# Kernel tuning notes

Measured on AMD Instinct MI355X. Metric: run time of the kernel, lower is better.

Reference implementation:

```python
import jax, jax.numpy as jnp
import numpy as np

DIM = 1024      # dim
FW = 14         # focal_window
FL = 2          # focal_level
FF = 4          # focal_factor


def _dwconv_gelu(x, w, b):
    # x: [B, C, S], w: [C, 1, k] depthwise kernel, torch 'same' padding
    k = w.shape[-1]
    y = jax.lax.conv_general_dilated(
        x, w, window_strides=(1,), padding=[((k - 1) // 2, k // 2)],
        feature_group_count=x.shape[1], dimension_numbers=('NCH', 'OIH', 'NCH'))
    return jax.nn.gelu(y + b[None, :, None], approximate=False)


def setup_inputs() -> dict:
    key = jax.random.key(0)
    ks = jax.random.split(key, 8)
    B, S, D = 8, 4096, DIM
    P = 2 * D + FL + 1  # 2051
    s = 0.02
    return {
        'input': jax.random.normal(ks[0], (B, S, D), jnp.float32),
        'W_in': jax.random.normal(ks[1], (D, P), jnp.float32) * s,
        'b_in': jnp.zeros((P,), jnp.float32),
        'w0': jax.random.normal(ks[2], (D, 1, FW), jnp.float32) * s,
        'b0': jnp.zeros((D,), jnp.float32),
        'w1': jax.random.normal(ks[3], (D, 1, FF + FW), jnp.float32) * s,  # kernel 18
        'b1': jnp.zeros((D,), jnp.float32),
        'W_ctx': jax.random.normal(ks[4], (D, D), jnp.float32) * s,
        'b_ctx': jnp.zeros((D,), jnp.float32),
        'W_out': jax.random.normal(ks[5], (D, D), jnp.float32) * s,
        'b_out': jnp.zeros((D,), jnp.float32),
    }


def reference(input, W_in, b_in, w0, b0, w1, b1, W_ctx, b_ctx, W_out, b_out):
    D = DIM
    # in_proj then permute to channel-first [B, 2D+FL+1, S]
    proj = (input @ W_in + b_in).transpose(0, 2, 1)
    query = proj[:, :D]            # [B, D, S]
    ctx = proj[:, D:2 * D]         # [B, D, S]
    gates = proj[:, 2 * D:]        # [B, FL+1, S]
    # hierarchical depthwise conv pyramid (context fed through successive levels)
    c0 = _dwconv_gelu(ctx, w0, b0)
    c1 = _dwconv_gelu(c0, w1, b1)
    context_all = c0 * gates[:, 0:1] + c1 * gates[:, 1:2]
    # global context branch
    g = jax.nn.gelu(c1.mean(axis=-1), approximate=False)  # [B, D]
    context_all = context_all + g[..., None] * gates[:, FL:FL + 1]
    # context_proj is a 1x1 conv == per-position linear over channels
    modulator = jnp.einsum('oc,bcs->bos', W_ctx, context_all) + b_ctx[None, :, None]
    out = (query * modulator).transpose(0, 2, 1)  # [B, S, D]
    return out @ W_out + b_out
```

## Files before the change

kernel.cpp:

```cpp
#include <hip/hip_runtime.h>

#define DIMC 1024
#define BATCH 8
#define SEQ 4096
#define BS (BATCH*SEQ)
#define PCOL 2051

typedef unsigned short ushort_t;
typedef __attribute__((ext_vector_type(8))) short short8;
typedef __attribute__((ext_vector_type(4))) float f32x4;
typedef __attribute__((ext_vector_type(4))) unsigned short us4;

__device__ __forceinline__ float bf2f(ushort_t u) {
    union { unsigned u32; float f; } v; v.u32 = ((unsigned)u) << 16; return v.f;
}
__device__ __forceinline__ ushort_t f2bf(float f) {
    union { float f; unsigned u; } v; v.f = f;
    unsigned r = v.u + 0x7fffu + ((v.u >> 16) & 1u);
    return (ushort_t)(r >> 16);
}
__device__ __forceinline__ float gelu_exact(float x) {
    return 0.5f * x * (1.0f + erff(x * 0.7071067811865475f));
}
__device__ __forceinline__ void gld16(const ushort_t* g, ushort_t* l) {
    __builtin_amdgcn_global_load_lds(
        (const __attribute__((address_space(1))) unsigned int*)g,
        (__attribute__((address_space(3))) unsigned int*)l, 16, 0, 0);
}

__global__ void cvt_f32_bf16(const float* __restrict__ src, ushort_t* __restrict__ dst, int n) {
    int i = (blockIdx.x * 256 + threadIdx.x) * 4;
    if (i >= n) return;
    f32x4 v = *(const f32x4*)(src + i);
    us4 o;
    #pragma unroll
    for (int j = 0; j < 4; j++) o[j] = f2bf(v[j]);
    *(us4*)(dst + i) = o;
}

__global__ void transpose_cvt(const float* __restrict__ src, ushort_t* __restrict__ dst,
                              int ld, int K) {
    __shared__ float tile[32][33];
    int tx = threadIdx.x & 31, ty = threadIdx.x >> 5;
    int n0 = blockIdx.x * 32, k0 = blockIdx.y * 32;
    #pragma unroll
    for (int j = 0; j < 4; j++)
        tile[ty + j * 8][tx] = src[(size_t)(k0 + ty + j * 8) * ld + n0 + tx];
    __syncthreads();
    #pragma unroll
    for (int j = 0; j < 4; j++)
        dst[(size_t)(n0 + ty + j * 8) * K + k0 + tx] = f2bf(tile[tx][ty + j * 8]);
}

__global__ void pack_gatesw(const float* __restrict__ W_in, float* __restrict__ wg) {
    int d = blockIdx.x * 256 + threadIdx.x;
    if (d >= 1024) return;
    const float* p = W_in + (size_t)d * PCOL + 2048;
    wg[d] = p[0]; wg[1024 + d] = p[1]; wg[2048 + d] = p[2];
}

__global__ void cvt_gates(const float* __restrict__ input, const float* __restrict__ wg,
                          const float* __restrict__ b_in, ushort_t* __restrict__ ibf,
                          float* __restrict__ gates) {
    int row = blockIdx.x, tid = threadIdx.x;
    int lane = tid & 63, wave = tid >> 6;
    size_t base = (size_t)row * 1024 + tid * 4;
    f32x4 v = *(const f32x4*)(input + base);
    us4 o;
    #pragma unroll
    for (int j = 0; j < 4; j++) o[j] = f2bf(v[j]);
    *(us4*)(ibf + base) = o;
    f32x4 w0v = *(const f32x4*)(wg + tid * 4);
    f32x4 w1v = *(const f32x4*)(wg + 1024 + tid * 4);
    f32x4 w2v = *(const f32x4*)(wg + 2048 + tid * 4);
    float a0 = 0, a1 = 0, a2 = 0;
    #pragma unroll
    for (int j = 0; j < 4; j++) { a0 += v[j] * w0v[j]; a1 += v[j] * w1v[j]; a2 += v[j] * w2v[j]; }
    #pragma unroll
    for (int off = 32; off; off >>= 1) {
        a0 += __shfl_down(a0, off, 64);
        a1 += __shfl_down(a1, off, 64);
        a2 += __shfl_down(a2, off, 64);
    }
    __shared__ float red[4][3];
    if (lane == 0) { red[wave][0] = a0; red[wave][1] = a1; red[wave][2] = a2; }
    __syncthreads();
    if (tid == 0) {
        gates[row * 4 + 0] = red[0][0] + red[1][0] + red[2][0] + red[3][0] + b_in[2048];
        gates[row * 4 + 1] = red[0][1] + red[1][1] + red[2][1] + red[3][1] + b_in[2049];
        gates[row * 4 + 2] = red[0][2] + red[1][2] + red[2][2] + red[3][2] + b_in[2050];
    }
}

template<int MODE>
__global__ __launch_bounds__(512, 2)
void gemm256(const ushort_t* __restrict__ A, const ushort_t* __restrict__ Bt,
             const float* __restrict__ bias, void* __restrict__ C,
             const ushort_t* __restrict__ Q, const float* __restrict__ gates,
             const float* __restrict__ vb, int K, int ldc, int ldq, int nbx) {
    __shared__ ushort_t lA[2][16384];
    __shared__ ushort_t lB[2][16384];
    const int tid = threadIdx.x, lane = tid & 63, wave = tid >> 6;
    const int lr = lane & 15, kq = lane >> 4;
    const int wrm = wave >> 2, wrn = wave & 3;

    const int nwg = gridDim.x, bid = blockIdx.x;
    const int q8 = nwg >> 3, r8 = nwg & 7;
    const int xcd = bid & 7, linb = bid >> 3;
    const int wgid = (xcd < r8 ? xcd * (q8 + 1) : r8 * (q8 + 1) + (xcd - r8) * q8) + linb;
    const int bn = wgid % nbx, bm = wgid / nbx;

    const ushort_t* Ag = A + (size_t)bm * 256 * K;
    const ushort_t* Bg = Bt + (size_t)bn * 256 * K;

    const int xsw = kq ^ (((lr >> 3) & 1) << 1);
    const int fBase = lr * 32 + xsw * 8;

    int srOff[2][2], ldsC[2][2];
    #pragma unroll
    for (int h = 0; h < 2; h++)
        #pragma unroll
        for (int j = 0; j < 2; j++) {
            int c = h * 1024 + j * 512 + tid;
            int sub = c >> 6, rl = (c >> 2) & 15, cc = c & 3;
            int r  = ((sub >> 1) << 4) | rl;
            int k8 = ((sub & 1) << 2) | (cc ^ (((rl >> 3) & 1) << 1));
            srOff[h][j] = r * K + k8 * 8;
            ldsC[h][j]  = (h * 1024 + j * 512 + (wave << 6)) << 3;
        }

    f32x4 acc[8][4];
    #pragma unroll
    for (int i = 0; i < 8; i++)
        #pragma unroll
        for (int j = 0; j < 4; j++)
            #pragma unroll
            for (int r = 0; r < 4; r++) acc[i][j][r] = 0.f;

    short8 af[2][2], bfr[4][2];

#define STG(ARR, bb, G, kt, h) do { \
    gld16((G) + (size_t)(kt) * 64 + srOff[h][0], &ARR[bb][ldsC[h][0]]); \
    gld16((G) + (size_t)(kt) * 64 + srOff[h][1], &ARR[bb][ldsC[h][1]]); \
} while (0)

#define PHASE(bb, qq, STAGE_STMT, DOVM) do { \
    if ((qq) == 0) { \
        _Pragma("unroll") \
        for (int nt = 0; nt < 4; nt++) { \
            bfr[nt][0] = *(const short8*)&lB[bb][fBase + ((wrn * 4 + nt) * 2 + 0) * 512]; \
            bfr[nt][1] = *(const short8*)&lB[bb][fBase + ((wrn * 4 + nt) * 2 + 1) * 512]; \
        } \
    } \
    af[0][0] = *(const short8*)&lA[bb][fBase + ((wrm * 8 + (qq) * 2 + 0) * 2 + 0) * 512]; \
    af[0][1] = *(const short8*)&lA[bb][fBase + ((wrm * 8 + (qq) * 2 + 0) * 2 + 1) * 512]; \
    af[1][0] = *(const short8*)&lA[bb][fBase + ((wrm * 8 + (qq) * 2 + 1) * 2 + 0) * 512]; \
    af[1][1] = *(const short8*)&lA[bb][fBase + ((wrm * 8 + (qq) * 2 + 1) * 2 + 1) * 512]; \
    STAGE_STMT; \
    __builtin_amdgcn_s_barrier(); \
    asm volatile("s_waitcnt lgkmcnt(0)" ::: "memory"); \
    __builtin_amdgcn_s_setprio(1); \
    _Pragma("unroll") \
    for (int mi = 0; mi < 2; mi++) \
        _Pragma("unroll") \
        for (int nt = 0; nt < 4; nt++) { \
            acc[(qq) * 2 + mi][nt] = __builtin_amdgcn_mfma_f32_16x16x32_bf16( \
                af[mi][0], bfr[nt][0], acc[(qq) * 2 + mi][nt], 0, 0, 0); \
            acc[(qq) * 2 + mi][nt] = __builtin_amdgcn_mfma_f32_16x16x32_bf16( \
                af[mi][1], bfr[nt][1], acc[(qq) * 2 + mi][nt], 0, 0, 0); \
        } \
    __builtin_amdgcn_s_setprio(0); \
    if (DOVM) asm volatile("s_waitcnt vmcnt(4)" ::: "memory"); \
    __builtin_amdgcn_s_barrier(); \
} while (0)

    STG(lA, 0, Ag, 0, 0); STG(lA, 0, Ag, 0, 1);
    STG(lB, 0, Bg, 0, 0); STG(lB, 0, Bg, 0, 1);
    STG(lB, 1, Bg, 1, 0); STG(lB, 1, Bg, 1, 1);
    asm volatile("s_waitcnt vmcnt(4)" ::: "memory");
    __builtin_amdgcn_s_barrier();

    const int KT = K >> 6;
    for (int it = 0; it < (K >> 7); it++) {
        int t1 = 2 * it + 1;
        int t2 = 2 * it + 2; if (t2 > KT - 1) t2 = KT - 1;
        int t3 = 2 * it + 3; if (t3 > KT - 1) t3 = KT - 1;
        PHASE(0, 0, STG(lA, 1, Ag, t1, 0), 0);
        PHASE(0, 1, STG(lA, 1, Ag, t1, 1), 0);
        PHASE(0, 2, STG(lB, 0, Bg, t2, 0), 0);
        PHASE(0, 3, STG(lB, 0, Bg, t2, 1), 1);
        PHASE(1, 0, STG(lA, 0, Ag, t2, 0), 0);
        PHASE(1, 1, STG(lA, 0, Ag, t2, 1), 0);
        PHASE(1, 2, STG(lB, 1, Bg, t3, 0), 0);
        PHASE(1, 3, STG(lB, 1, Bg, t3, 1), 1);
    }
#undef PHASE
#undef STG
    asm volatile("s_waitcnt vmcnt(0)" ::: "memory");

    const int bbatch = (bm * 256) >> 12;
    #pragma unroll
    for (int mt = 0; mt < 8; mt++) {
        #pragma unroll
        for (int r = 0; r < 4; r++) {
            int row = bm * 256 + wrm * 128 + mt * 16 + kq * 4 + r;
            size_t rowc = (size_t)row * ldc;
            float g2;
            if (MODE == 1) g2 = gates[row * 4 + 2];
            #pragma unroll
            for (int nt = 0; nt < 4; nt++) {
                int col = bn * 256 + wrn * 64 + nt * 16 + lr;
                float v = acc[mt][nt][r] + bias[col];
                if (MODE == 1) {
                    v += g2 * vb[bbatch * 1024 + col];
                    v *= bf2f(Q[(size_t)row * ldq + col]);
                }
                if (MODE == 2) ((float*)C)[rowc + col] = v;
                else           ((ushort_t*)C)[rowc + col] = f2bf(v);
            }
        }
    }
}

__global__ __launch_bounds__(256)
void dwconv_fused(const ushort_t* __restrict__ proj,
                  const float* __restrict__ w0, const float* __restrict__ b0,
                  const float* __restrict__ w1, const float* __restrict__ b1,
                  const float* __restrict__ gates,
                  ushort_t* __restrict__ P, float* __restrict__ G) {
    __shared__ float xc[94 * 64];
    __shared__ float x0[81 * 64];
    __shared__ float gl[2][64];
    __shared__ float rs[256];
    const int tid = threadIdx.x;
    const int s0 = blockIdx.x * 64, d0 = blockIdx.y * 64, b = blockIdx.z;
    for (int c = tid; c < 94 * 8; c += 256) {
        int r = c >> 3, dd = (c & 7) * 8;
        int s = s0 - 14 + r;
        float f[8];
        if (s >= 0 && s < SEQ) {
            short8 u = *(const short8*)&proj[(size_t)(b * SEQ + s) * 2048 + 1024 + d0 + dd];
            #pragma unroll
            for (int j = 0; j < 8; j++) f[j] = bf2f((ushort_t)u[j]);
        } else {
            #pragma unroll
            for (int j = 0; j < 8; j++) f[j] = 0.f;
        }
        f32x4 v0 = {f[0], f[1], f[2], f[3]}, v1 = {f[4], f[5], f[6], f[7]};
        *(f32x4*)&xc[r * 64 + dd] = v0;
        *(f32x4*)&xc[r * 64 + dd + 4] = v1;
    }
    if (tid < 64) gl[0][tid] = gates[(size_t)(b * SEQ + s0 + tid) * 4 + 0];
    else if (tid < 128) gl[1][tid - 64] = gates[(size_t)(b * SEQ + s0 + tid - 64) * 4 + 1];
    const int d = tid & 63, sc = tid >> 6;
    float wr0[14], wr1[18];
    #pragma unroll
    for (int t = 0; t < 14; t++) wr0[t] = w0[(size_t)(d0 + d) * 14 + t];
    float bb0 = b0[d0 + d];
    #pragma unroll
    for (int t = 0; t < 18; t++) wr1[t] = w1[(size_t)(d0 + d) * 18 + t];
    float bb1 = b1[d0 + d];
    __syncthreads();
    {
        float xw[34];
        int r0 = sc * 20;
        #pragma unroll
        for (int r = 0; r < 34; r++) xw[r] = xc[(r0 + r) * 64 + d];
        #pragma unroll
        for (int i = 0; i < 21; i++) {
            int rr = r0 + i;
            int s = s0 - 8 + rr;
            float acc = bb0;
            #pragma unroll
            for (int t = 0; t < 14; t++) acc += wr0[t] * xw[i + t];
            x0[rr * 64 + d] = (s >= 0 && s < SEQ) ? gelu_exact(acc) : 0.f;
        }
    }
    __syncthreads();
    float xw1[33];
    #pragma unroll
    for (int r = 0; r < 33; r++) xw1[r] = x0[(sc * 16 + r) * 64 + d];
    float psum = 0.f;
    #pragma unroll
    for (int i = 0; i < 16; i++) {
        float acc = bb1;
        #pragma unroll
        for (int t = 0; t < 18; t++) acc += wr1[t] * xw1[i + t];
        float c1 = gelu_exact(acc);
        psum += c1;
        float c0v = xw1[i + 8];
        int sl = sc * 16 + i;
        float pv = c0v * gl[0][sl] + c1 * gl[1][sl];
        P[(size_t)(b * SEQ + s0 + sl) * 1024 + d0 + d] = f2bf(pv);
    }
    rs[tid] = psum;
    __syncthreads();
    if (sc == 0)
        atomicAdd(&G[b * 1024 + d0 + d], rs[d] + rs[64 + d] + rs[128 + d] + rs[192 + d]);
}

__global__ __launch_bounds__(256)
void gemv_v(const float* __restrict__ G, const ushort_t* __restrict__ wctxB,
            float* __restrict__ v) {
    __shared__ float gg[1024];
    const int tid = threadIdx.x, b = blockIdx.y;
    for (int i = tid; i < 1024; i += 256)
        gg[i] = gelu_exact(G[b * 1024 + i] * (1.0f / (float)SEQ));
    __syncthreads();
    const int w = tid >> 6, lane = tid & 63;
    const int o = blockIdx.x * 4 + w;
    const ushort_t* wr = wctxB + (size_t)o * 1024;
    float acc = 0.f;
    #pragma unroll
    for (int j = 0; j < 16; j++)
        acc += gg[j * 64 + lane] * bf2f(wr[j * 64 + lane]);
    #pragma unroll
    for (int off = 32; off; off >>= 1) acc += __shfl_down(acc, off, 64);
    if (lane == 0) v[b * 1024 + o] = acc;
}

extern "C" void kernel_launch(void* const* d_in, const int* in_sizes, int n_in,
                              void* d_out, int out_size, void* d_ws, size_t ws_size,
                              hipStream_t stream) {
    const float* input = (const float*)d_in[0];
    const float* W_in  = (const float*)d_in[1];
    const float* b_in  = (const float*)d_in[2];
    const float* w0    = (const float*)d_in[3];
    const float* b0    = (const float*)d_in[4];
    const float* w1    = (const float*)d_in[5];
    const float* b1    = (const float*)d_in[6];
    const float* W_ctx = (const float*)d_in[7];
    const float* b_ctx = (const float*)d_in[8];
    const float* W_out = (const float*)d_in[9];
    const float* b_out = (const float*)d_in[10];

    char* ws = (char*)d_ws;
    size_t o = 0;
    ushort_t* ibf   = (ushort_t*)(ws + o); o += (size_t)BS * 1024 * 2;
    ushort_t* proj  = (ushort_t*)(ws + o); o += (size_t)BS * 2048 * 2;
    ushort_t* Y     = (ushort_t*)(ws + o); o += (size_t)BS * 1024 * 2;
    float*    gates = (float*)   (ws + o); o += (size_t)BS * 4 * 4;
    float*    G     = (float*)   (ws + o); o += (size_t)BATCH * 1024 * 4;
    float*    v     = (float*)   (ws + o); o += (size_t)BATCH * 1024 * 4;
    float*    wg    = (float*)   (ws + o); o += (size_t)3 * 1024 * 4;
    ushort_t* winT  = (ushort_t*)(ws + o); o += (size_t)2048 * 1024 * 2;
    ushort_t* wctxB = (ushort_t*)(ws + o); o += (size_t)1024 * 1024 * 2;
    ushort_t* woutT = (ushort_t*)(ws + o); o += (size_t)1024 * 1024 * 2;
    ushort_t* P = ibf;

    hipMemsetAsync(G, 0, BATCH * 1024 * sizeof(float), stream);
    pack_gatesw<<<4, 256, 0, stream>>>(W_in, wg);
    transpose_cvt<<<dim3(2048 / 32, 1024 / 32), 256, 0, stream>>>(W_in, winT, PCOL, 1024);
    cvt_f32_bf16<<<1024 * 1024 / 4 / 256, 256, 0, stream>>>(W_ctx, wctxB, 1024 * 1024);
    transpose_cvt<<<dim3(1024 / 32, 1024 / 32), 256, 0, stream>>>(W_out, woutT, 1024, 1024);
    cvt_gates<<<BS, 256, 0, stream>>>(input, wg, b_in, ibf, gates);
    gemm256<0><<<dim3(8 * (BS / 256)), 512, 0, stream>>>(ibf, winT, b_in, proj,
        nullptr, nullptr, nullptr, 1024, 2048, 0, 8);
    dwconv_fused<<<dim3(SEQ / 64, 16, BATCH), 256, 0, stream>>>(proj, w0, b0, w1, b1, gates, P, G);
    gemv_v<<<dim3(256, BATCH), 256, 0, stream>>>(G, wctxB, v);
    gemm256<1><<<dim3(4 * (BS / 256)), 512, 0, stream>>>(P, wctxB, b_ctx, Y,
        proj, gates, v, 1024, 1024, 2048, 4);
    gemm256<2><<<dim3(4 * (BS / 256)), 512, 0, stream>>>(Y, woutT, b_out, d_out,
        nullptr, nullptr, nullptr, 1024, 1024, 0, 4);
}
```

Baseline: 660.8 us.

## Make GEMM kernels persistent and prefetch the next tile during the tail

Converts the three bf16 GEMM launches into persistent kernels with a 256-block grid, where each block processes a contiguous run of output tiles (4 for in_proj, 2 for the others). Prefetches of the next tile's first K slices are issued during the last K iterations of the current tile, so global loads overlap the epilogue and the next tile's prologue. Tiles are assigned per XCD in contiguous chunks. This removes the wave-quantization tail and per-block launch/prologue cost, in exchange for less scheduling flexibility and the epilogue stores now sitting on the critical path between tiles.

```diff
diff --git a/kernel.cpp b/kernel.cpp
--- a/kernel.cpp
+++ b/kernel.cpp
@@ -97,21 +97,16 @@
 void gemm256(const ushort_t* __restrict__ A, const ushort_t* __restrict__ Bt,
              const float* __restrict__ bias, void* __restrict__ C,
              const ushort_t* __restrict__ Q, const float* __restrict__ gates,
-             const float* __restrict__ vb, int K, int ldc, int ldq, int nbx) {
+             const float* __restrict__ vb, int K, int ldc, int ldq, int nbx, int tpb) {
     __shared__ ushort_t lA[2][16384];
     __shared__ ushort_t lB[2][16384];
     const int tid = threadIdx.x, lane = tid & 63, wave = tid >> 6;
     const int lr = lane & 15, kq = lane >> 4;
     const int wrm = wave >> 2, wrn = wave & 3;
 
-    const int nwg = gridDim.x, bid = blockIdx.x;
-    const int q8 = nwg >> 3, r8 = nwg & 7;
-    const int xcd = bid & 7, linb = bid >> 3;
-    const int wgid = (xcd < r8 ? xcd * (q8 + 1) : r8 * (q8 + 1) + (xcd - r8) * q8) + linb;
-    const int bn = wgid % nbx, bm = wgid / nbx;
-
-    const ushort_t* Ag = A + (size_t)bm * 256 * K;
-    const ushort_t* Bg = Bt + (size_t)bn * 256 * K;
+    const int bid = blockIdx.x;
+    const int chunk = (gridDim.x >> 3) * tpb;
+    const int tile0 = (bid & 7) * chunk + (bid >> 3) * tpb;
 
     const int xsw = kq ^ (((lr >> 3) & 1) << 1);
     const int fBase = lr * 32 + xsw * 8;
@@ -130,13 +125,6 @@
         }
 
     f32x4 acc[8][4];
-    #pragma unroll
-    for (int i = 0; i < 8; i++)
-        #pragma unroll
-        for (int j = 0; j < 4; j++)
-            #pragma unroll
-            for (int r = 0; r < 4; r++) acc[i][j][r] = 0.f;
-
     short8 af[2][2], bfr[4][2];
 
 #define STG(ARR, bb, G, kt, h) do { \
@@ -174,52 +162,81 @@
     __builtin_amdgcn_s_barrier(); \
 } while (0)
 
+    const int KT = K >> 6;
+    const int IT = K >> 7;
+
+    int j = tile0;
+    int bn = j % nbx, bm = j / nbx;
+    const ushort_t* Ag = A + (size_t)bm * 256 * K;
+    const ushort_t* Bg = Bt + (size_t)bn * 256 * K;
+
     STG(lA, 0, Ag, 0, 0); STG(lA, 0, Ag, 0, 1);
     STG(lB, 0, Bg, 0, 0); STG(lB, 0, Bg, 0, 1);
     STG(lB, 1, Bg, 1, 0); STG(lB, 1, Bg, 1, 1);
     asm volatile("s_waitcnt vmcnt(4)" ::: "memory");
     __builtin_amdgcn_s_barrier();
 
-    const int KT = K >> 6;
-    for (int it = 0; it < (K >> 7); it++) {
-        int t1 = 2 * it + 1;
-        int t2 = 2 * it + 2; if (t2 > KT - 1) t2 = KT - 1;
-        int t3 = 2 * it + 3; if (t3 > KT - 1) t3 = KT - 1;
-        PHASE(0, 0, STG(lA, 1, Ag, t1, 0), 0);
-        PHASE(0, 1, STG(lA, 1, Ag, t1, 1), 0);
-        PHASE(0, 2, STG(lB, 0, Bg, t2, 0), 0);
-        PHASE(0, 3, STG(lB, 0, Bg, t2, 1), 1);
-        PHASE(1, 0, STG(lA, 0, Ag, t2, 0), 0);
-        PHASE(1, 1, STG(lA, 0, Ag, t2, 1), 0);
-        PHASE(1, 2, STG(lB, 1, Bg, t3, 0), 0);
-        PHASE(1, 3, STG(lB, 1, Bg, t3, 1), 1);
+    for (int ti = 0; ti < tpb; ti++) {
+        const int jn = (ti < tpb - 1) ? j + 1 : j;
+        const int bnn = jn % nbx, bmn = jn / nbx;
+        const ushort_t* Agn = A + (size_t)bmn * 256 * K;
+        const ushort_t* Bgn = Bt + (size_t)bnn * 256 * K;
+
+        #pragma unroll
+        for (int i = 0; i < 8; i++)
+            #pragma unroll
+            for (int jj = 0; jj < 4; jj++)
+                #pragma unroll
+                for (int r = 0; r < 4; r++) acc[i][jj][r] = 0.f;
+
+        for (int it = 0; it < IT - 1; it++) {
+            const int t1 = 2 * it + 1, t2 = 2 * it + 2, t3 = 2 * it + 3;
+            PHASE(0, 0, STG(lA, 1, Ag, t1, 0), 0);
+            PHASE(0, 1, STG(lA, 1, Ag, t1, 1), 0);
+            PHASE(0, 2, STG(lB, 0, Bg, t2, 0), 0);
+            PHASE(0, 3, STG(lB, 0, Bg, t2, 1), 1);
+            PHASE(1, 0, STG(lA, 0, Ag, t2, 0), 0);
+            PHASE(1, 1, STG(lA, 0, Ag, t2, 1), 0);
+            PHASE(1, 2, STG(lB, 1, Bg, t3, 0), 0);
+            PHASE(1, 3, STG(lB, 1, Bg, t3, 1), 1);
+        }
+        PHASE(0, 0, STG(lA, 1, Ag, KT - 1, 0), 0);
+        PHASE(0, 1, STG(lA, 1, Ag, KT - 1, 1), 0);
+        PHASE(0, 2, STG(lB, 0, Bgn, 0, 0), 0);
+        PHASE(0, 3, STG(lB, 0, Bgn, 0, 1), 1);
+        PHASE(1, 0, STG(lA, 0, Agn, 0, 0), 0);
+        PHASE(1, 1, STG(lA, 0, Agn, 0, 1), 0);
+        PHASE(1, 2, STG(lB, 1, Bgn, 1, 0), 0);
+        PHASE(1, 3, STG(lB, 1, Bgn, 1, 1), 1);
+
+        const int bbatch = (bm * 256) >> 12;
+        #pragma unroll
+        for (int mt = 0; mt < 8; mt++) {
+            #pragma unroll
+            for (int r = 0; r < 4; r++) {
+                int row = bm * 256 + wrm * 128 + mt * 16 + kq * 4 + r;
+                size_t rowc = (size_t)row * ldc;
+                float g2;
+                if (MODE == 1) g2 = gates[row * 4 + 2];
+                #pragma unroll
+                for (int nt = 0; nt < 4; nt++) {
+                    int col = bn * 256 + wrn * 64 + nt * 16 + lr;
+                    float v = acc[mt][nt][r] + bias[col];
+                    if (MODE == 1) {
+                        v += g2 * vb[bbatch * 1024 + col];
+                        v *= bf2f(Q[(size_t)row * ldq + col]);
+                    }
+                    if (MODE == 2) ((float*)C)[rowc + col] = v;
+                    else           ((ushort_t*)C)[rowc + col] = f2bf(v);
+                }
+            }
+        }
+
+        j = jn; bm = bmn; bn = bnn; Ag = Agn; Bg = Bgn;
     }
 #undef PHASE
 #undef STG
-    asm volatile("s_waitcnt vmcnt(0)" ::: "memory");
-
-    const int bbatch = (bm * 256) >> 12;
-    #pragma unroll
-    for (int mt = 0; mt < 8; mt++) {
-        #pragma unroll
-        for (int r = 0; r < 4; r++) {
-            int row = bm * 256 + wrm * 128 + mt * 16 + kq * 4 + r;
-            size_t rowc = (size_t)row * ldc;
-            float g2;
-            if (MODE == 1) g2 = gates[row * 4 + 2];
-            #pragma unroll
-            for (int nt = 0; nt < 4; nt++) {
-                int col = bn * 256 + wrn * 64 + nt * 16 + lr;
-                float v = acc[mt][nt][r] + bias[col];
-                if (MODE == 1) {
-                    v += g2 * vb[bbatch * 1024 + col];
-                    v *= bf2f(Q[(size_t)row * ldq + col]);
-                }
-                if (MODE == 2) ((float*)C)[rowc + col] = v;
-                else           ((ushort_t*)C)[rowc + col] = f2bf(v);
-            }
-        }
-    }
+    asm volatile("s_waitcnt vmcnt(0) lgkmcnt(0)" ::: "memory");
 }
 
 __global__ __launch_bounds__(256)
@@ -354,12 +371,12 @@
     cvt_f32_bf16<<<1024 * 1024 / 4 / 256, 256, 0, stream>>>(W_ctx, wctxB, 1024 * 1024);
     transpose_cvt<<<dim3(1024 / 32, 1024 / 32), 256, 0, stream>>>(W_out, woutT, 1024, 1024);
     cvt_gates<<<BS, 256, 0, stream>>>(input, wg, b_in, ibf, gates);
-    gemm256<0><<<dim3(8 * (BS / 256)), 512, 0, stream>>>(ibf, winT, b_in, proj,
-        nullptr, nullptr, nullptr, 1024, 2048, 0, 8);
+    gemm256<0><<<dim3(256), 512, 0, stream>>>(ibf, winT, b_in, proj,
+        nullptr, nullptr, nullptr, 1024, 2048, 0, 8, 4);
     dwconv_fused<<<dim3(SEQ / 64, 16, BATCH), 256, 0, stream>>>(proj, w0, b0, w1, b1, gates, P, G);
     gemv_v<<<dim3(256, BATCH), 256, 0, stream>>>(G, wctxB, v);
-    gemm256<1><<<dim3(4 * (BS / 256)), 512, 0, stream>>>(P, wctxB, b_ctx, Y,
-        proj, gates, v, 1024, 1024, 2048, 4);
-    gemm256<2><<<dim3(4 * (BS / 256)), 512, 0, stream>>>(Y, woutT, b_out, d_out,
-        nullptr, nullptr, nullptr, 1024, 1024, 0, 4);
-}
+    gemm256<1><<<dim3(256), 512, 0, stream>>>(P, wctxB, b_ctx, Y,
+        proj, gates, v, 1024, 1024, 2048, 4, 2);
+    gemm256<2><<<dim3(256), 512, 0, stream>>>(Y, woutT, b_out, d_out,
+        nullptr, nullptr, nullptr, 1024, 1024, 0, 4, 2);
+}
```

New measurement: 669.3 us. About the same (+1.3%).
